# Kernel tuning notes

Hardware: AMD Instinct MI355X
Metric: run time of the kernel (lower is better)

Reference implementation:

```python
import jax, jax.numpy as jnp
import numpy as np

BITS = 4
MAXQ = (1 << BITS) - 1  # 15
PACK = 32 // BITS       # 8 nibbles per int32


def setup_inputs() -> dict:
    key = jax.random.key(0)
    k = jax.random.split(key, 6)
    B, S, IN, OUT, G = 4, 2048, 4096, 4096, 32
    groups = IN // G  # 128
    imin, imax = np.iinfo(np.int32).min, np.iinfo(np.int32).max
    x = jax.random.normal(k[0], (B, S, IN), dtype=jnp.float32)
    qweight = jax.random.randint(k[1], (IN // PACK, OUT), imin, imax, dtype=jnp.int32)
    qzeros = jax.random.randint(k[2], (groups, OUT // PACK), imin, imax, dtype=jnp.int32)
    qscales = jax.random.randint(k[3], (groups, OUT, 1), 0, 256, dtype=jnp.int32)
    qscales_zeros = jax.random.uniform(k[4], (groups, 1, 1), dtype=jnp.float32)
    qscales_scales = jax.random.uniform(k[5], (groups, 1, 1), dtype=jnp.float32) * 0.01
    g_idx = (jnp.arange(IN, dtype=jnp.int32) // G)
    return {"x": x, "qweight": qweight, "qzeros": qzeros, "qscales": qscales,
            "qscales_zeros": qscales_zeros, "qscales_scales": qscales_scales, "g_idx": g_idx}


def reference(x, qweight, qzeros, qscales, qscales_zeros, qscales_scales, g_idx):
    out_features = qweight.shape[-1]
    shifts = jnp.arange(0, 32, BITS, dtype=jnp.int32)  # (8,)
    # --- unpack int4 weights: (in/8, 8, out) -> (in, out); mask makes arith shift == logical
    w = (qweight[:, None, :] >> shifts[None, :, None]) & MAXQ
    w = w.reshape(-1, out_features)  # (in, out), values 0..15
    # --- unpack zeros: (groups, out/8, 8) -> (groups, out); +1 per original
    z = ((qzeros[:, :, None] >> shifts[None, None, :]) & MAXQ) + 1
    z = z.reshape(qzeros.shape[0], -1)  # (groups, out)
    z = z[g_idx]  # (in, out)
    # --- double-dequant scales: (groups, out, 1) with (groups, 1, 1) stats
    scales = (qscales.astype(x.dtype) - qscales_zeros) * qscales_scales
    scales = scales.reshape(qscales.shape[0], -1)[g_idx]  # (in, out)
    weight = ((w - z) * scales).astype(x.dtype)  # (in, out)
    return jnp.matmul(x, weight)
```

## Files before the change

kernel.cpp:

```cpp
#include <hip/hip_runtime.h>

typedef __attribute__((ext_vector_type(8))) short short8;
typedef __attribute__((ext_vector_type(4))) float floatx4;
typedef unsigned int u32;
typedef unsigned short u16;

__device__ __forceinline__ u16 f2bf(float f) {
  u32 u = __float_as_uint(f);
  u += 0x7FFFu + ((u >> 16) & 1u);
  return (u16)(u >> 16);
}

typedef const __attribute__((address_space(1))) u32* gp1_t;
typedef __attribute__((address_space(3))) u32* lp3_t;

__device__ __forceinline__ void gld16(const void* g, void* l) {
  __builtin_amdgcn_global_load_lds((gp1_t)g, (lp3_t)l, 16, 0, 0);
}

__global__ __launch_bounds__(256) void xconv(const float* __restrict__ x,
                                             u16* __restrict__ xb, long long n4) {
  long long i = (long long)blockIdx.x * 256 + threadIdx.x;
  if (i >= n4) return;
  float4 v = ((const float4*)x)[i];
  ushort4 o;
  o.x = f2bf(v.x); o.y = f2bf(v.y); o.z = f2bf(v.z); o.w = f2bf(v.w);
  ((ushort4*)xb)[i] = o;
}

__global__ __launch_bounds__(256) void dequant(
    const int* __restrict__ qw, const int* __restrict__ qz,
    const int* __restrict__ qs, const float* __restrict__ qsz,
    const float* __restrict__ qss, const int* __restrict__ gidx,
    u16* __restrict__ Wt, int IN, int OUT) {
  const int n = blockIdx.x * 64 + (threadIdx.x & 63);
  const int w = threadIdx.x >> 6;
  const int k0 = blockIdx.y * 128 + w * 32;
  const int g = gidx[k0];
  const int kk0 = k0 >> 3;
  const int zq = ((qz[(size_t)g * (OUT >> 3) + (n >> 3)] >> (4 * (n & 7))) & 15) + 1;
  const float sc = ((float)qs[(size_t)g * OUT + n] - qsz[g]) * qss[g];
  u16* dst = Wt + (size_t)n * IN + k0;
#pragma unroll
  for (int j = 0; j < 4; ++j) {
    const int w32 = qw[(size_t)(kk0 + j) * OUT + n];
    u16 o[8];
#pragma unroll
    for (int s = 0; s < 8; ++s)
      o[s] = f2bf((float)(((w32 >> (4 * s)) & 15) - zq) * sc);
    uint4 pk;
    pk.x = (u32)o[0] | ((u32)o[1] << 16);
    pk.y = (u32)o[2] | ((u32)o[3] << 16);
    pk.z = (u32)o[4] | ((u32)o[5] << 16);
    pk.w = (u32)o[6] | ((u32)o[7] << 16);
    *(uint4*)(dst + j * 8) = pk;
  }
}

#define VM4 asm volatile("s_waitcnt vmcnt(4)" ::: "memory")
#define VM0 asm volatile("s_waitcnt vmcnt(0)" ::: "memory")

__global__ __launch_bounds__(512, 2) void gemm256(const u16* __restrict__ A,
                                                  const u16* __restrict__ Bt,
                                                  float* __restrict__ C,
                                                  int M, int N, int K) {
  __shared__ u16 As[2][16384];
  __shared__ u16 Bs[2][16384];
  const int tid = threadIdx.x;
  const int lane = tid & 63;
  const int wave = tid >> 6;
  const int wm = wave >> 2;
  const int wn = wave & 3;
  const int lr = lane & 15, quad = lane >> 4;

  const int nbx = N >> 8;
  const int nwg = gridDim.x;
  const int bid = blockIdx.x;
  const int q8 = nwg >> 3, r8 = nwg & 7;
  const int xcd = bid & 7, loc = bid >> 3;
  const int swz = (xcd < r8 ? xcd * (q8 + 1) : r8 * (q8 + 1) + (xcd - r8) * q8) + loc;
  const int n0 = (swz % nbx) << 8;
  const int m0 = (swz / nbx) << 8;

  floatx4 acc[8][4] = {};

  const int srow = lane >> 3;
  const int sch8 = ((lane & 7) ^ (srow & 7)) * 8;
  const u16* aS = A + (size_t)(m0 + wave * 8 + srow) * K + sch8;
  const u16* bS = Bt + (size_t)(n0 + wave * 8 + srow) * K + sch8;

#define STAGE_A(buf, h, kt) do {                                              \
    const u16* s_ = aS + (size_t)(h) * 128 * K + (size_t)(kt) * 64;           \
    u16* d_ = &As[buf][((h) * 128 + wave * 8) * 64];                          \
    gld16(s_, d_); gld16(s_ + (size_t)64 * K, d_ + 4096);                     \
  } while (0)
#define STAGE_B(buf, h, kt) do {                                              \
    const u16* s_ = bS + (size_t)(h) * 128 * K + (size_t)(kt) * 64;           \
    u16* d_ = &Bs[buf][((h) * 128 + wave * 8) * 64];                          \
    gld16(s_, d_); gld16(s_ + (size_t)64 * K, d_ + 4096);                     \
  } while (0)

  const int rl = lr & 7;
  const int cs0 = ((0 * 4 + quad) ^ rl) * 8;
  const int cs1 = ((1 * 4 + quad) ^ rl) * 8;
  const u16* a0rd = &As[0][(wm * 128 + lr) * 64];
  const u16* a1rd = &As[1][(wm * 128 + lr) * 64];
  const u16* b0rd = &Bs[0][(wn * 64 + lr) * 64];
  const u16* b1rd = &Bs[1][(wn * 64 + lr) * 64];

  short8 aF[2][2], bF[4][2];

#define PHASE(ARD, BRD, q, LOADB, STG, VMW) do {                              \
    if (LOADB) {                                                              \
      _Pragma("unroll") for (int nt = 0; nt < 4; ++nt) {                      \
        bF[nt][0] = *(const short8*)((BRD) + nt * 1024 + cs0);                \
        bF[nt][1] = *(const short8*)((BRD) + nt * 1024 + cs1);                \
      }                                                                       \
    }                                                                         \
    aF[0][0] = *(const short8*)((ARD) + (2 * (q)) * 1024 + cs0);              \
    aF[0][1] = *(const short8*)((ARD) + (2 * (q)) * 1024 + cs1);              \
    aF[1][0] = *(const short8*)((ARD) + (2 * (q) + 1) * 1024 + cs0);          \
    aF[1][1] = *(const short8*)((ARD) + (2 * (q) + 1) * 1024 + cs1);          \
    STG;                                                                      \
    __builtin_amdgcn_s_barrier();                                             \
    __builtin_amdgcn_s_setprio(1);                                            \
    _Pragma("unroll") for (int s = 0; s < 2; ++s)                             \
      _Pragma("unroll") for (int j = 0; j < 2; ++j)                           \
        _Pragma("unroll") for (int nt = 0; nt < 4; ++nt)                      \
          acc[2 * (q) + j][nt] = __builtin_amdgcn_mfma_f32_16x16x32_bf16(     \
              aF[j][s], bF[nt][s], acc[2 * (q) + j][nt], 0, 0, 0);            \
    __builtin_amdgcn_s_setprio(0);                                            \
    VMW;                                                                      \
    __builtin_amdgcn_s_barrier();                                             \
  } while (0)

  STAGE_B(0, 0, 0); STAGE_B(0, 1, 0);
  STAGE_A(0, 0, 0); STAGE_A(0, 1, 0);
  STAGE_B(1, 0, 1); STAGE_B(1, 1, 1);
  VM4;
  __builtin_amdgcn_s_barrier();

  const int NI = K >> 7;
  for (int i = 0; i < NI; ++i) {
    const int kt = 2 * i;
    const bool full = (i < NI - 1);
    PHASE(a0rd, b0rd, 0, 1, { STAGE_A(1, 0, kt + 1); }, (void)0);
    PHASE(a0rd, b0rd, 1, 0, { STAGE_A(1, 1, kt + 1); }, (void)0);
    PHASE(a0rd, b0rd, 2, 0, { if (full) STAGE_B(0, 0, kt + 2); }, (void)0);
    PHASE(a0rd, b0rd, 3, 0, { if (full) STAGE_B(0, 1, kt + 2); },
          { if (full) { VM4; } else { VM0; } });
    PHASE(a1rd, b1rd, 0, 1, { if (full) STAGE_A(0, 0, kt + 2); }, (void)0);
    PHASE(a1rd, b1rd, 1, 0, { if (full) STAGE_A(0, 1, kt + 2); }, (void)0);
    PHASE(a1rd, b1rd, 2, 0, { if (full) STAGE_B(1, 0, kt + 3); }, (void)0);
    PHASE(a1rd, b1rd, 3, 0, { if (full) STAGE_B(1, 1, kt + 3); },
          { if (full) { VM4; } });
  }
#undef PHASE
#undef STAGE_A
#undef STAGE_B

#pragma unroll
  for (int mt = 0; mt < 8; ++mt)
#pragma unroll
    for (int nt = 0; nt < 4; ++nt)
#pragma unroll
      for (int r = 0; r < 4; ++r) {
        int row = m0 + wm * 128 + mt * 16 + quad * 4 + r;
        int col = n0 + wn * 64 + nt * 16 + lr;
        C[(size_t)row * N + col] = acc[mt][nt][r];
      }
}

__global__ __launch_bounds__(256) void gemm(const u16* __restrict__ A,
                                            const u16* __restrict__ Bt,
                                            float* __restrict__ C,
                                            int M, int N, int K) {
  __shared__ u16 As[128 * 64];
  __shared__ u16 Bs[128 * 64];
  const int tid = threadIdx.x;
  const int lane = tid & 63;
  const int wave = tid >> 6;
  const int wm = wave & 1, wn = wave >> 1;
  const int lr = lane & 15, quad = lane >> 4;
  const int m0 = blockIdx.y * 128, n0 = blockIdx.x * 128;

  floatx4 acc[4][4] = {};

  const int srowB = (lane >> 3);
  const int schunk = (lane & 7) ^ srowB;
  const int rowA0 = wave * 32;
  const u16* aSrc = A + (size_t)(m0 + rowA0 + srowB) * K + schunk * 8;
  const u16* bSrc = Bt + (size_t)(n0 + rowA0 + srowB) * K + schunk * 8;
  u16* aDst = &As[rowA0 * 64];
  u16* bDst = &Bs[rowA0 * 64];
  const size_t rstep = (size_t)8 * K;

  const int rx = lr & 7;

  for (int k0 = 0; k0 < K; k0 += 64) {
    __syncthreads();
#pragma unroll
    for (int c = 0; c < 4; ++c) {
      gld16(aSrc + c * rstep + k0, aDst + c * 8 * 64);
      gld16(bSrc + c * rstep + k0, bDst + c * 8 * 64);
    }
    __syncthreads();

#pragma unroll
    for (int h = 0; h < 2; ++h) {
      short8 aF[4], bF[4];
      const int rc = ((quad + 4 * h) ^ rx) * 8;
#pragma unroll
      for (int t = 0; t < 4; ++t) {
        aF[t] = *(const short8*)&As[(wm * 64 + t * 16 + lr) * 64 + rc];
        bF[t] = *(const short8*)&Bs[(wn * 64 + t * 16 + lr) * 64 + rc];
      }
#pragma unroll
      for (int mt = 0; mt < 4; ++mt)
#pragma unroll
        for (int nt = 0; nt < 4; ++nt)
          acc[mt][nt] = __builtin_amdgcn_mfma_f32_16x16x32_bf16(
              aF[mt], bF[nt], acc[mt][nt], 0, 0, 0);
    }
  }

#pragma unroll
  for (int mt = 0; mt < 4; ++mt)
#pragma unroll
    for (int nt = 0; nt < 4; ++nt)
#pragma unroll
      for (int r = 0; r < 4; ++r) {
        int row = m0 + wm * 64 + mt * 16 + quad * 4 + r;
        int col = n0 + wn * 64 + nt * 16 + lr;
        C[(size_t)row * N + col] = acc[mt][nt][r];
      }
}

__global__ void naive(const float* __restrict__ x, const int* __restrict__ qw,
                      const int* __restrict__ qz, const int* __restrict__ qs,
                      const float* __restrict__ qsz, const float* __restrict__ qss,
                      const int* __restrict__ gidx, float* __restrict__ out,
                      int M, int N, int K) {
  int n = blockIdx.x * 64 + (threadIdx.x & 63);
  int m = blockIdx.y * 4 + (threadIdx.x >> 6);
  if (n >= N || m >= M) return;
  float acc = 0.f;
  for (int kk = 0; kk < K / 8; ++kk) {
    int w32 = qw[(size_t)kk * N + n];
#pragma unroll
    for (int s = 0; s < 8; ++s) {
      int k = kk * 8 + s;
      int g = gidx[k];
      int zq = ((qz[(size_t)g * (N >> 3) + (n >> 3)] >> (4 * (n & 7))) & 15) + 1;
      float sc = ((float)qs[(size_t)g * N + n] - qsz[g]) * qss[g];
      acc += x[(size_t)m * K + k] * ((float)((w32 >> (4 * s)) & 15) - (float)zq) * sc;
    }
  }
  out[(size_t)m * N + n] = acc;
}

extern "C" void kernel_launch(void* const* d_in, const int* in_sizes, int n_in,
                              void* d_out, int out_size, void* d_ws, size_t ws_size,
                              hipStream_t stream) {
  const float* x = (const float*)d_in[0];
  const int* qw = (const int*)d_in[1];
  const int* qz = (const int*)d_in[2];
  const int* qs = (const int*)d_in[3];
  const float* qsz = (const float*)d_in[4];
  const float* qss = (const float*)d_in[5];
  const int* gidx = (const int*)d_in[6];
  const int IN = in_sizes[6];
  const int OUT = (int)(((long long)in_sizes[1] * 8) / IN);
  const int M = in_sizes[0] / IN;
  float* out = (float*)d_out;

  size_t bytesW = (size_t)IN * OUT * 2;
  size_t bytesX = (size_t)M * IN * 2;
  bool haveWs = (ws_size >= bytesW + bytesX);
  bool fast256 = haveWs && (M % 256 == 0) && (OUT % 256 == 0) &&
                 (IN % 128 == 0) && (IN >= 256);
  bool fast128 = haveWs && (M % 128 == 0) && (OUT % 128 == 0) && (IN % 128 == 0);

  if (fast256 || fast128) {
    u16* Wt = (u16*)d_ws;
    u16* Xb = (u16*)((char*)d_ws + bytesW);
    long long n4 = (long long)M * IN / 4;
    int cb = (int)((n4 + 255) / 256);
    xconv<<<cb, 256, 0, stream>>>(x, Xb, n4);
    dequant<<<dim3(OUT / 64, IN / 128), 256, 0, stream>>>(qw, qz, qs, qsz, qss,
                                                          gidx, Wt, IN, OUT);
    if (fast256) {
      int nblk = (M / 256) * (OUT / 256);
      gemm256<<<dim3(nblk), 512, 0, stream>>>(Xb, Wt, out, M, OUT, IN);
    } else {
      gemm<<<dim3(OUT / 128, M / 128), 256, 0, stream>>>(Xb, Wt, out, M, OUT, IN);
    }
  } else {
    naive<<<dim3((OUT + 63) / 64, (M + 3) / 4), 256, 0, stream>>>(
        x, qw, qz, qs, qsz, qss, gidx, out, M, OUT, IN);
  }
}
```

Baseline: 489.8 us.

## Switch bf16 GEMM from 16x16x32 to 32x32x16 MFMA tiles

Reworks the 256x256 tile GEMM so each wave computes with 32x32x16 bf16 MFMA instructions instead of 16x16x32. Fragment loading, LDS swizzle offsets, the accumulator layout and the output store mapping change to match. The pipeline drops from four phases per buffer to two, each issuing two staged loads. The aim is fewer LDS fragment reads per FLOP and fewer MFMA issues. The cost is more live registers per phase and coarser load/compute interleaving.

```diff
diff --git a/kernel.cpp b/kernel.cpp
--- a/kernel.cpp
+++ b/kernel.cpp
@@ -2,6 +2,7 @@
 
 typedef __attribute__((ext_vector_type(8))) short short8;
 typedef __attribute__((ext_vector_type(4))) float floatx4;
+typedef __attribute__((ext_vector_type(16))) float f32x16;
 typedef unsigned int u32;
 typedef unsigned short u16;
 
@@ -71,7 +72,7 @@
   const int wave = tid >> 6;
   const int wm = wave >> 2;
   const int wn = wave & 3;
-  const int lr = lane & 15, quad = lane >> 4;
+  const int l31 = lane & 31, hi = lane >> 5, l7 = lane & 7;
 
   const int nbx = N >> 8;
   const int nwg = gridDim.x;
@@ -82,7 +83,7 @@
   const int n0 = (swz % nbx) << 8;
   const int m0 = (swz / nbx) << 8;
 
-  floatx4 acc[8][4] = {};
+  f32x16 acc[4][2] = {};
 
   const int srow = lane >> 3;
   const int sch8 = ((lane & 7) ^ (srow & 7)) * 8;
@@ -100,35 +101,33 @@
     gld16(s_, d_); gld16(s_ + (size_t)64 * K, d_ + 4096);                     \
   } while (0)
 
-  const int rl = lr & 7;
-  const int cs0 = ((0 * 4 + quad) ^ rl) * 8;
-  const int cs1 = ((1 * 4 + quad) ^ rl) * 8;
-  const u16* a0rd = &As[0][(wm * 128 + lr) * 64];
-  const u16* a1rd = &As[1][(wm * 128 + lr) * 64];
-  const u16* b0rd = &Bs[0][(wn * 64 + lr) * 64];
-  const u16* b1rd = &Bs[1][(wn * 64 + lr) * 64];
-
-  short8 aF[2][2], bF[4][2];
+  int ko[4];
+#pragma unroll
+  for (int ks = 0; ks < 4; ++ks) ko[ks] = ((ks * 2 + hi) ^ l7) * 8;
+  const u16* a0rd = &As[0][(wm * 128 + l31) * 64];
+  const u16* a1rd = &As[1][(wm * 128 + l31) * 64];
+  const u16* b0rd = &Bs[0][(wn * 64 + l31) * 64];
+  const u16* b1rd = &Bs[1][(wn * 64 + l31) * 64];
+
+  short8 aF[2][4], bF[2][4];
 
 #define PHASE(ARD, BRD, q, LOADB, STG, VMW) do {                              \
     if (LOADB) {                                                              \
-      _Pragma("unroll") for (int nt = 0; nt < 4; ++nt) {                      \
-        bF[nt][0] = *(const short8*)((BRD) + nt * 1024 + cs0);                \
-        bF[nt][1] = *(const short8*)((BRD) + nt * 1024 + cs1);                \
-      }                                                                       \
+      _Pragma("unroll") for (int nt = 0; nt < 2; ++nt)                        \
+        _Pragma("unroll") for (int ks = 0; ks < 4; ++ks)                      \
+          bF[nt][ks] = *(const short8*)((BRD) + nt * 2048 + ko[ks]);          \
     }                                                                         \
-    aF[0][0] = *(const short8*)((ARD) + (2 * (q)) * 1024 + cs0);              \
-    aF[0][1] = *(const short8*)((ARD) + (2 * (q)) * 1024 + cs1);              \
-    aF[1][0] = *(const short8*)((ARD) + (2 * (q) + 1) * 1024 + cs0);          \
-    aF[1][1] = *(const short8*)((ARD) + (2 * (q) + 1) * 1024 + cs1);          \
+    _Pragma("unroll") for (int j = 0; j < 2; ++j)                             \
+      _Pragma("unroll") for (int ks = 0; ks < 4; ++ks)                        \
+        aF[j][ks] = *(const short8*)((ARD) + (2 * (q) + j) * 2048 + ko[ks]);  \
     STG;                                                                      \
     __builtin_amdgcn_s_barrier();                                             \
     __builtin_amdgcn_s_setprio(1);                                            \
-    _Pragma("unroll") for (int s = 0; s < 2; ++s)                             \
+    _Pragma("unroll") for (int ks = 0; ks < 4; ++ks)                          \
       _Pragma("unroll") for (int j = 0; j < 2; ++j)                           \
-        _Pragma("unroll") for (int nt = 0; nt < 4; ++nt)                      \
-          acc[2 * (q) + j][nt] = __builtin_amdgcn_mfma_f32_16x16x32_bf16(     \
-              aF[j][s], bF[nt][s], acc[2 * (q) + j][nt], 0, 0, 0);            \
+        _Pragma("unroll") for (int nt = 0; nt < 2; ++nt)                      \
+          acc[2 * (q) + j][nt] = __builtin_amdgcn_mfma_f32_32x32x16_bf16(     \
+              aF[j][ks], bF[nt][ks], acc[2 * (q) + j][nt], 0, 0, 0);          \
     __builtin_amdgcn_s_setprio(0);                                            \
     VMW;                                                                      \
     __builtin_amdgcn_s_barrier();                                             \
@@ -144,15 +143,16 @@
   for (int i = 0; i < NI; ++i) {
     const int kt = 2 * i;
     const bool full = (i < NI - 1);
-    PHASE(a0rd, b0rd, 0, 1, { STAGE_A(1, 0, kt + 1); }, (void)0);
-    PHASE(a0rd, b0rd, 1, 0, { STAGE_A(1, 1, kt + 1); }, (void)0);
-    PHASE(a0rd, b0rd, 2, 0, { if (full) STAGE_B(0, 0, kt + 2); }, (void)0);
-    PHASE(a0rd, b0rd, 3, 0, { if (full) STAGE_B(0, 1, kt + 2); },
+    PHASE(a0rd, b0rd, 0, 1, { STAGE_A(1, 0, kt + 1); STAGE_A(1, 1, kt + 1); },
+          (void)0);
+    PHASE(a0rd, b0rd, 1, 0,
+          { if (full) { STAGE_B(0, 0, kt + 2); STAGE_B(0, 1, kt + 2); } },
           { if (full) { VM4; } else { VM0; } });
-    PHASE(a1rd, b1rd, 0, 1, { if (full) STAGE_A(0, 0, kt + 2); }, (void)0);
-    PHASE(a1rd, b1rd, 1, 0, { if (full) STAGE_A(0, 1, kt + 2); }, (void)0);
-    PHASE(a1rd, b1rd, 2, 0, { if (full) STAGE_B(1, 0, kt + 3); }, (void)0);
-    PHASE(a1rd, b1rd, 3, 0, { if (full) STAGE_B(1, 1, kt + 3); },
+    PHASE(a1rd, b1rd, 0, 1,
+          { if (full) { STAGE_A(0, 0, kt + 2); STAGE_A(0, 1, kt + 2); } },
+          (void)0);
+    PHASE(a1rd, b1rd, 1, 0,
+          { if (full) { STAGE_B(1, 0, kt + 3); STAGE_B(1, 1, kt + 3); } },
           { if (full) { VM4; } });
   }
 #undef PHASE
@@ -160,13 +160,13 @@
 #undef STAGE_B
 
 #pragma unroll
-  for (int mt = 0; mt < 8; ++mt)
-#pragma unroll
-    for (int nt = 0; nt < 4; ++nt)
-#pragma unroll
-      for (int r = 0; r < 4; ++r) {
-        int row = m0 + wm * 128 + mt * 16 + quad * 4 + r;
-        int col = n0 + wn * 64 + nt * 16 + lr;
+  for (int mt = 0; mt < 4; ++mt)
+#pragma unroll
+    for (int nt = 0; nt < 2; ++nt)
+#pragma unroll
+      for (int r = 0; r < 16; ++r) {
+        int row = m0 + wm * 128 + mt * 32 + (r & 3) + 8 * (r >> 2) + 4 * hi;
+        int col = n0 + wn * 64 + nt * 32 + l31;
         C[(size_t)row * N + col] = acc[mt][nt][r];
       }
 }
```

Measured after the change: 512.5 us. +4.7%, slower.
